# Performance work log

Hardware: AMD Instinct MI355X
Metric: run time of the kernel (lower is better)

Reference implementation:

```python
import jax, jax.numpy as jnp
import numpy as np
import math

B, T, C = 4, 2048, 1024
H, D = 16, 64            # num_heads, head_dim
ORIG_LEN = 4096
MIN_FREQ, MAX_FREQ = 0.5, 40.0


def setup_inputs() -> dict:
    key = jax.random.key(0)
    ks = jax.random.split(key, 6)
    x = jax.random.normal(ks[0], (B, T, C), dtype=jnp.float32)
    keep_idx = jnp.sort(jax.random.randint(ks[1], (B, T, 1), 0, ORIG_LEN), axis=1)
    W_qkv = jax.random.normal(ks[2], (C, 3 * C), dtype=jnp.float32) * (1.0 / math.sqrt(C))
    b_qkv = jnp.zeros((3 * C,), dtype=jnp.float32)
    W_proj = jax.random.normal(ks[3], (C, C), dtype=jnp.float32) * (1.0 / math.sqrt(C))
    b_proj = jnp.zeros((C,), dtype=jnp.float32)
    return {"x": x, "keep_idx": keep_idx, "original_seq_len": ORIG_LEN,
            "W_qkv": W_qkv, "b_qkv": b_qkv, "W_proj": W_proj, "b_proj": b_proj}


def _rope_angles(positions, orig_len):
    # positions: [b, t] float token positions in the ORIGINAL sequence.
    # golden_gate 1-D RoPE: normalized positions times geometric frequency band.
    half = D // 2
    freqs = MIN_FREQ * (MAX_FREQ / MIN_FREQ) ** (jnp.arange(half, dtype=jnp.float32) / (half - 1))
    pos_norm = positions / jnp.float32(orig_len)          # [b, t]
    return 2.0 * jnp.pi * pos_norm[:, :, None] * freqs    # [b, t, half]


def _apply_rope(x, cos, sin):
    # x: [b, h, t, d]; cos/sin: [b, 1, t, d/2]; rotate (first half, second half) pairs
    half = D // 2
    x1, x2 = x[..., :half], x[..., half:]
    return jnp.concatenate([x1 * cos - x2 * sin, x1 * sin + x2 * cos], axis=-1)


def reference(x, keep_idx, original_seq_len, W_qkv, b_qkv, W_proj, b_proj):
    b, t, c = x.shape
    # fused QKV projection + head split: (b,t,3c) -> (b,t,3,h,d) -> (b,h,t,3,d)
    qkv = (x @ W_qkv + b_qkv).reshape(b, t, 3, H, D).transpose(0, 3, 1, 2, 4)
    q, k, v = qkv[:, :, :, 0], qkv[:, :, :, 1], qkv[:, :, :, 2]  # each [b,h,t,d]

    positions = keep_idx[..., 0].astype(jnp.float32)             # [b, t]
    ang = _rope_angles(positions, original_seq_len)              # [b, t, d/2]
    cos = jnp.cos(ang)[:, None]                                  # [b,1,t,d/2]
    sin = jnp.sin(ang)[:, None]
    q = _apply_rope(q, cos, sin)
    k = _apply_rope(k, cos, sin)

    # dense non-causal scaled dot-product attention
    scale = 1.0 / math.sqrt(D)
    scores = jnp.einsum('bhqd,bhkd->bhqk', q, k) * scale
    attn = jax.nn.softmax(scores, axis=-1)
    out = jnp.einsum('bhqk,bhkd->bhqd', attn, v)                 # [b,h,t,d]

    out = out.transpose(0, 2, 1, 3).reshape(b, t, H * D)         # [b,t,c]
    return out @ W_proj + b_proj
```

## Files before the change

### kernel.cpp

```cpp
#include <hip/hip_runtime.h>
#include <hip/hip_bf16.h>
#include <math.h>

#define B_ 4
#define T_ 2048
#define C_ 1024
#define H_ 16
#define D_ 64

typedef __attribute__((ext_vector_type(8))) short bf16x8_t;
typedef __attribute__((ext_vector_type(4))) float f32x4_t;
typedef __attribute__((ext_vector_type(2))) unsigned int uiv2_t;

#define SHIFT2 32.0f

#define GLOAD_LDS16(gp, lp)                                                          \
    __builtin_amdgcn_global_load_lds(                                                \
        (const __attribute__((address_space(1))) void*)(gp),                         \
        (__attribute__((address_space(3))) void*)(lp), 16, 0, 0)

#define WAVE_ORDER() __builtin_amdgcn_wave_barrier()

__device__ inline short bf16bits(float f) {
    __hip_bfloat16 h = __float2bfloat16(f);
    return *reinterpret_cast<short*>(&h);
}

__device__ inline unsigned int pack2bf(float a, float b) {
    __hip_bfloat162 h = __float22bfloat162_rn(make_float2(a, b));
    return *reinterpret_cast<unsigned int*>(&h);
}

__global__ void xconv_kernel(const float* __restrict__ in,
                             __hip_bfloat16* __restrict__ out, int n4) {
    int i = blockIdx.x * blockDim.x + threadIdx.x;
    if (i < n4) {
        float4 v = *(const float4*)(in + (size_t)i * 4);
        uint2 u;
        u.x = pack2bf(v.x, v.y);
        u.y = pack2bf(v.z, v.w);
        *(uint2*)(out + (size_t)i * 4) = u;
    }
}

__global__ void rope_tab_kernel(const int* __restrict__ keep,
                                const int* __restrict__ orig,
                                float* __restrict__ tab) {
    int i = blockIdx.x * blockDim.x + threadIdx.x;
    int tok = i >> 5, d = i & 31;
    float freq = 0.5f * exp2f((float)d * (6.321928094887362f / 31.0f));
    float ang  = 6.283185307179586f * ((float)keep[tok] / (float)(*orig)) * freq;
    tab[(size_t)tok * 64 + d]      = cosf(ang);
    tab[(size_t)tok * 64 + 32 + d] = sinf(ang);
}

__global__ void transpose_conv_kernel(const float* __restrict__ in,
                                      __hip_bfloat16* __restrict__ out,
                                      int K, int N) {
    __shared__ float s[32][33];
    const int n0 = blockIdx.x * 32;
    const int k0 = blockIdx.y * 32;
    const int tx = threadIdx.x;
    const int ty = threadIdx.y;
#pragma unroll
    for (int yy = 0; yy < 32; yy += 8)
        s[ty + yy][tx] = in[(size_t)(k0 + ty + yy) * N + n0 + tx];
    __syncthreads();
#pragma unroll
    for (int yy = 0; yy < 32; yy += 8)
        out[(size_t)(n0 + ty + yy) * K + k0 + tx] = __float2bfloat16(s[tx][ty + yy]);
}

#define GTILE (128 * 32)

template <int MODE>
__global__ __launch_bounds__(256)
void gemm_kernel(const __hip_bfloat16* __restrict__ A,
                 const __hip_bfloat16* __restrict__ BT,
                 const float* __restrict__ bias,
                 float* __restrict__ out,
                 __hip_bfloat16* __restrict__ qbuf,
                 __hip_bfloat16* __restrict__ kbuf,
                 __hip_bfloat16* __restrict__ vtbuf,
                 const float* __restrict__ ropetab,
                 int M, int N, int K) {
    __shared__ __align__(16) __hip_bfloat16 As[2 * GTILE];
    __shared__ __align__(16) __hip_bfloat16 Bs[2 * GTILE];

    const int tid  = threadIdx.x;
    const int lane = tid & 63;
    const int wave = tid >> 6;
    const int wm   = wave >> 1;
    const int wn   = wave & 1;
    const int l15  = lane & 15;
    const int quad = lane >> 4;

    const int nT  = N >> 7;
    const int grp = blockIdx.x / (8 * nT);
    const int rem = blockIdx.x - grp * 8 * nT;
    const int m0  = (grp * 8 + (rem & 7)) * 128;
    const int n0  = (rem >> 3) * 128;

    f32x4_t acc[4][4];
#pragma unroll
    for (int i = 0; i < 4; i++)
#pragma unroll
        for (int j = 0; j < 4; j++) acc[i][j] = (f32x4_t)0.0f;

    const int lrow = lane >> 2;
    const int lcol = (lane & 3) * 8;
    const __hip_bfloat16* gA  = A  + (size_t)(m0 + wave * 16 + lrow) * K + lcol;
    const __hip_bfloat16* gA2 = gA + (size_t)64 * K;
    const __hip_bfloat16* gB  = BT + (size_t)(n0 + wave * 16 + lrow) * K + lcol;
    const __hip_bfloat16* gB2 = gB + (size_t)64 * K;
    const int ldsW = wave * 16 * 32;

    GLOAD_LDS16(gA,  As + ldsW);
    GLOAD_LDS16(gA2, As + ldsW + 64 * 32);
    GLOAD_LDS16(gB,  Bs + ldsW);
    GLOAD_LDS16(gB2, Bs + ldsW + 64 * 32);

    const int NK = K >> 5;
    for (int t = 0; t < NK; ++t) {
        const int off = (t & 1) * GTILE;
        if (t + 1 < NK) {
            const int noff = off ^ GTILE;
            const int kk   = (t + 1) << 5;
            GLOAD_LDS16(gA  + kk, As + noff + ldsW);
            GLOAD_LDS16(gA2 + kk, As + noff + ldsW + 64 * 32);
            GLOAD_LDS16(gB  + kk, Bs + noff + ldsW);
            GLOAD_LDS16(gB2 + kk, Bs + noff + ldsW + 64 * 32);
            asm volatile("s_waitcnt vmcnt(4)" ::: "memory");
        } else {
            asm volatile("s_waitcnt vmcnt(0)" ::: "memory");
        }
        __builtin_amdgcn_s_barrier();
        __builtin_amdgcn_sched_barrier(0);

        bf16x8_t af[4], bfv[4];
#pragma unroll
        for (int i = 0; i < 4; i++)
            af[i] = *(const bf16x8_t*)(As + off + (wm * 64 + i * 16 + l15) * 32 + quad * 8);
#pragma unroll
        for (int j = 0; j < 4; j++)
            bfv[j] = *(const bf16x8_t*)(Bs + off + (wn * 64 + j * 16 + l15) * 32 + quad * 8);
#pragma unroll
        for (int i = 0; i < 4; i++)
#pragma unroll
            for (int j = 0; j < 4; j++)
                acc[i][j] = __builtin_amdgcn_mfma_f32_16x16x32_bf16(af[i], bfv[j], acc[i][j], 0, 0, 0);

        __builtin_amdgcn_sched_barrier(0);
        asm volatile("s_waitcnt lgkmcnt(0)" ::: "memory");
        __builtin_amdgcn_s_barrier();
    }

    float bv[4];
#pragma unroll
    for (int j = 0; j < 4; j++)
        bv[j] = bias[n0 + wn * 64 + j * 16 + l15];

    if (MODE == 0) {
#pragma unroll
        for (int i = 0; i < 4; i++)
#pragma unroll
            for (int r = 0; r < 4; r++) {
                int row = m0 + wm * 64 + i * 16 + quad * 4 + r;
#pragma unroll
                for (int j = 0; j < 4; j++) {
                    int col = n0 + wn * 64 + j * 16 + l15;
                    out[(size_t)row * N + col] = acc[i][j][r] + bv[j];
                }
            }
    } else {
        const int cb   = n0 + wn * 64;
        const int part = cb >> 10;
        const int h    = (cb & 1023) >> 6;
        if (part == 2) {
#pragma unroll
            for (int j = 0; j < 4; j++) {
#pragma unroll
                for (int i = 0; i < 4; i++) {
#pragma unroll
                    for (int r = 0; r < 4; r++) {
                        int row = m0 + wm * 64 + i * 16 + quad * 4 + r;
                        int b = row >> 11;
                        int t = row & 2047;
                        int d = j * 16 + l15;
                        vtbuf[((size_t)((b * H_ + h) * D_ + d)) * T_ + t] =
                            __float2bfloat16(acc[i][j][r] + bv[j]);
                    }
                }
            }
        } else {
            __hip_bfloat16* dst = (part == 0) ? qbuf : kbuf;
            const float sc = (part == 0) ? 0.18033688011112042f : 1.0f;
#pragma unroll
            for (int i = 0; i < 4; i++) {
#pragma unroll
                for (int r = 0; r < 4; r++) {
                    int row = m0 + wm * 64 + i * 16 + quad * 4 + r;
                    int b = row >> 11;
                    int t = row & 2047;
                    const float* trow = ropetab + (size_t)row * 64;
                    size_t base = ((size_t)(b * H_ + h) * T_ + t) * D_;
#pragma unroll
                    for (int j = 0; j < 2; j++) {
                        int d = j * 16 + l15;
                        float cs = trow[d];
                        float sn = trow[32 + d];
                        float x1 = acc[i][j][r]     + bv[j];
                        float x2 = acc[i][j + 2][r] + bv[j + 2];
                        dst[base + d]      = __float2bfloat16(sc * (x1 * cs - x2 * sn));
                        dst[base + d + 32] = __float2bfloat16(sc * (x1 * sn + x2 * cs));
                    }
                }
            }
        }
    }
}

#define KVTILE (64 * 64)

__global__ __launch_bounds__(256, 4)
void attn_kernel(const __hip_bfloat16* __restrict__ q,
                 const __hip_bfloat16* __restrict__ k,
                 const __hip_bfloat16* __restrict__ vt,
                 __hip_bfloat16* __restrict__ attn_out) {
    __shared__ __align__(16) __hip_bfloat16 SMEM[4 * KVTILE];

    const int tid  = threadIdx.x;
    const int lane = tid & 63;
    const int wave = tid >> 6;
    const int l15  = lane & 15;
    const int quad = lane >> 4;
    const int x7   = l15 & 7;

    const int bh = blockIdx.x & 63;
    const int qt = blockIdx.x >> 6;
    const int b  = bh >> 4;
    const int h  = bh & 15;

    const size_t qkbase = (size_t)bh * T_ * D_;
    const size_t vbase  = (size_t)bh * D_ * T_;
    const int    qrow0  = qt * 128 + wave * 32;

    const int drow   = lane >> 3;
    const int gchunk = (lane & 7) ^ drow;

    const __hip_bfloat16* kg = k + qkbase;
    const __hip_bfloat16* vg = vt + vbase;

    const int c0 = ((quad)     ^ x7) * 8;
    const int c1 = ((4 + quad) ^ x7) * 8;

    bf16x8_t qa[2][2];
#pragma unroll
    for (int qf = 0; qf < 2; qf++)
#pragma unroll
        for (int kk = 0; kk < 2; kk++)
            qa[qf][kk] = *(const bf16x8_t*)(q + qkbase +
                          (size_t)(qrow0 + qf * 16 + l15) * D_ + kk * 32 + quad * 8);

    bf16x8_t ones;
#pragma unroll
    for (int i = 0; i < 8; i++) ones[i] = (short)0x3F80;

    const f32x4_t mbias = (f32x4_t)(-SHIFT2);

    f32x4_t o[2][4];
#pragma unroll
    for (int qf = 0; qf < 2; qf++)
#pragma unroll
        for (int jd = 0; jd < 4; jd++) o[qf][jd] = (f32x4_t)0.0f;
    f32x4_t osum[2];
    osum[0] = (f32x4_t)0.0f;
    osum[1] = (f32x4_t)0.0f;

#pragma unroll
    for (int i = 0; i < 2; i++) {
        int r = wave * 16 + i * 8;
        GLOAD_LDS16(kg + (size_t)(r + drow) * D_ + gchunk * 8, SMEM + r * 64);
        GLOAD_LDS16(vg + (size_t)(r + drow) * T_ + gchunk * 8, SMEM + 2 * KVTILE + r * 64);
    }

    for (int kt = 0; kt < T_ / 64; kt++) {
        const int curoff = (kt & 1) * KVTILE;
        const int nxtoff = curoff ^ KVTILE;
        if (kt + 1 < T_ / 64) {
#pragma unroll
            for (int i = 0; i < 2; i++) {
                int r = wave * 16 + i * 8;
                GLOAD_LDS16(kg + (size_t)((kt + 1) * 64 + r + drow) * D_ + gchunk * 8,
                            SMEM + nxtoff + r * 64);
                GLOAD_LDS16(vg + (size_t)(r + drow) * T_ + (kt + 1) * 64 + gchunk * 8,
                            SMEM + 2 * KVTILE + nxtoff + r * 64);
            }
            asm volatile("s_waitcnt vmcnt(4)" ::: "memory");
        } else {
            asm volatile("s_waitcnt vmcnt(0)" ::: "memory");
        }
        __builtin_amdgcn_s_barrier();
        __builtin_amdgcn_sched_barrier(0);

        const __hip_bfloat16* KLc = SMEM + curoff;
        const __hip_bfloat16* VLc = SMEM + 2 * KVTILE + curoff;

        bf16x8_t kf[4][2];
#pragma unroll
        for (int jt = 0; jt < 4; jt++) {
            kf[jt][0] = *(const bf16x8_t*)(KLc + (jt * 16 + l15) * 64 + c0);
            kf[jt][1] = *(const bf16x8_t*)(KLc + (jt * 16 + l15) * 64 + c1);
        }

        f32x4_t sT[2][4];
        __builtin_amdgcn_s_setprio(1);
#pragma unroll
        for (int jt = 0; jt < 4; jt++)
#pragma unroll
            for (int qf = 0; qf < 2; qf++) {
                sT[qf][jt] = __builtin_amdgcn_mfma_f32_16x16x32_bf16(
                    kf[jt][0], qa[qf][0], mbias, 0, 0, 0);
                sT[qf][jt] = __builtin_amdgcn_mfma_f32_16x16x32_bf16(
                    kf[jt][1], qa[qf][1], sT[qf][jt], 0, 0, 0);
            }
        __builtin_amdgcn_s_setprio(0);

        bf16x8_t pb[2][2];
#pragma unroll
        for (int qf = 0; qf < 2; qf++) {
            unsigned int w0[4], w1[4];
#pragma unroll
            for (int jt = 0; jt < 4; jt++) {
                float p0 = __builtin_amdgcn_exp2f(sT[qf][jt][0]);
                float p1 = __builtin_amdgcn_exp2f(sT[qf][jt][1]);
                float p2 = __builtin_amdgcn_exp2f(sT[qf][jt][2]);
                float p3 = __builtin_amdgcn_exp2f(sT[qf][jt][3]);
                w0[jt] = pack2bf(p0, p1);
                w1[jt] = pack2bf(p2, p3);
            }
#pragma unroll
            for (int kk = 0; kk < 2; kk++) {
                uiv2_t s0 = __builtin_amdgcn_permlane32_swap(w0[2 * kk], w0[2 * kk + 1], false, false);
                uiv2_t r0 = __builtin_amdgcn_permlane16_swap(s0[0], s0[1], false, false);
                uiv2_t s1 = __builtin_amdgcn_permlane32_swap(w1[2 * kk], w1[2 * kk + 1], false, false);
                uiv2_t r1 = __builtin_amdgcn_permlane16_swap(s1[0], s1[1], false, false);
                union { unsigned int u[4]; bf16x8_t v; } pu;
                pu.u[0] = r0[0];
                pu.u[1] = r1[0];
                pu.u[2] = r0[1];
                pu.u[3] = r1[1];
                pb[qf][kk] = pu.v;
            }
        }

        __builtin_amdgcn_s_setprio(1);
#pragma unroll
        for (int qf = 0; qf < 2; qf++) {
            osum[qf] = __builtin_amdgcn_mfma_f32_16x16x32_bf16(ones, pb[qf][0], osum[qf], 0, 0, 0);
            osum[qf] = __builtin_amdgcn_mfma_f32_16x16x32_bf16(ones, pb[qf][1], osum[qf], 0, 0, 0);
        }

#pragma unroll
        for (int jd = 0; jd < 4; jd++) {
            bf16x8_t vf0 = *(const bf16x8_t*)(VLc + (jd * 16 + l15) * 64 + c0);
            bf16x8_t vf1 = *(const bf16x8_t*)(VLc + (jd * 16 + l15) * 64 + c1);
#pragma unroll
            for (int qf = 0; qf < 2; qf++) {
                o[qf][jd] = __builtin_amdgcn_mfma_f32_16x16x32_bf16(vf0, pb[qf][0], o[qf][jd], 0, 0, 0);
                o[qf][jd] = __builtin_amdgcn_mfma_f32_16x16x32_bf16(vf1, pb[qf][1], o[qf][jd], 0, 0, 0);
            }
        }
        __builtin_amdgcn_s_setprio(0);

        __builtin_amdgcn_sched_barrier(0);
        asm volatile("s_waitcnt lgkmcnt(0)" ::: "memory");
        __builtin_amdgcn_s_barrier();
    }

    float inv[2];
    inv[0] = 1.0f / osum[0][0];
    inv[1] = 1.0f / osum[1][0];

    __hip_bfloat16* Pep = SMEM + wave * (32 * 72);

    WAVE_ORDER();
#pragma unroll
    for (int qf = 0; qf < 2; qf++) {
#pragma unroll
        for (int jd = 0; jd < 4; jd++) {
            uint2 pk;
            pk.x = pack2bf(o[qf][jd][0] * inv[qf], o[qf][jd][1] * inv[qf]);
            pk.y = pack2bf(o[qf][jd][2] * inv[qf], o[qf][jd][3] * inv[qf]);
            *(uint2*)(Pep + (qf * 16 + l15) * 72 + jd * 16 + quad * 4) = pk;
        }
    }
    WAVE_ORDER();

#pragma unroll
    for (int rnd = 0; rnd < 4; rnd++) {
        int row = rnd * 8 + (lane >> 3);
        int col = (lane & 7) * 8;
        bf16x8_t vrow = *(const bf16x8_t*)(Pep + row * 72 + col);
        int token = qt * 128 + wave * 32 + row;
        *(bf16x8_t*)(attn_out + ((size_t)(b * T_ + token)) * C_ + h * 64 + col) = vrow;
    }
}

extern "C" void kernel_launch(void* const* d_in, const int* in_sizes, int n_in,
                              void* d_out, int out_size, void* d_ws, size_t ws_size,
                              hipStream_t stream) {
    const float* x        = (const float*)d_in[0];
    const int*   keep_idx = (const int*)d_in[1];
    const int*   orig_len = (const int*)d_in[2];
    const float* Wqkv     = (const float*)d_in[3];
    const float* bqkv     = (const float*)d_in[4];
    const float* Wproj    = (const float*)d_in[5];
    const float* bproj    = (const float*)d_in[6];
    float*       out      = (float*)d_out;

    const size_t NTOK = (size_t)B_ * T_;
    const size_t QKV1 = NTOK * C_;

    __hip_bfloat16* qbuf    = (__hip_bfloat16*)d_ws;
    __hip_bfloat16* kbuf    = qbuf    + QKV1;
    __hip_bfloat16* vtbuf   = kbuf    + QKV1;
    __hip_bfloat16* attnbuf = vtbuf   + QKV1;
    __hip_bfloat16* WqkvT   = attnbuf + QKV1;
    __hip_bfloat16* WprojT  = WqkvT   + (size_t)C_ * 3 * C_;
    __hip_bfloat16* xbf     = WprojT  + (size_t)C_ * C_;
    float*          ropetab = (float*)(xbf + QKV1);

    xconv_kernel<<<(QKV1 / 4 + 255) / 256, 256, 0, stream>>>(x, xbf, (int)(QKV1 / 4));
    rope_tab_kernel<<<(NTOK * 32) / 256, 256, 0, stream>>>(keep_idx, orig_len, ropetab);

    dim3 tb(32, 8);
    transpose_conv_kernel<<<dim3(3 * C_ / 32, C_ / 32), tb, 0, stream>>>(Wqkv, WqkvT, C_, 3 * C_);
    transpose_conv_kernel<<<dim3(C_ / 32, C_ / 32), tb, 0, stream>>>(Wproj, WprojT, C_, C_);

    gemm_kernel<1><<<(8192 / 128) * (3072 / 128), 256, 0, stream>>>(
        xbf, WqkvT, bqkv, nullptr, qbuf, kbuf, vtbuf, ropetab, 8192, 3072, 1024);

    attn_kernel<<<(T_ / 128) * 64, 256, 0, stream>>>(qbuf, kbuf, vtbuf, attnbuf);

    gemm_kernel<0><<<(8192 / 128) * (1024 / 128), 256, 0, stream>>>(
        attnbuf, WprojT, bproj, out, nullptr, nullptr, nullptr, nullptr, 8192, 1024, 1024);
}
```

Measured before the change: 296.8 us.

## Triple-buffer GEMM LDS with XOR swizzle and stage V-transpose through LDS

The GEMM main loop moves from double to triple buffering, so global-to-LDS loads run two k-tiles ahead with a deeper vmcnt wait. The LDS tile layout is XOR-swizzled on both the global_load_lds write side and the MFMA fragment read side to cut bank conflicts. The V-transpose epilogue now stages the tile in shared memory and writes vtbuf with contiguous 16-byte stores instead of strided scalar stores. LDS use grows from 4 to 6 tiles, which may lower occupancy, and the epilogue adds a block-wide sync.

```diff
diff --git a/kernel.cpp b/kernel.cpp
--- a/kernel.cpp
+++ b/kernel.cpp
@@ -84,8 +84,7 @@
                  __hip_bfloat16* __restrict__ vtbuf,
                  const float* __restrict__ ropetab,
                  int M, int N, int K) {
-    __shared__ __align__(16) __hip_bfloat16 As[2 * GTILE];
-    __shared__ __align__(16) __hip_bfloat16 Bs[2 * GTILE];
+    __shared__ __align__(16) __hip_bfloat16 GS[6 * GTILE];
 
     const int tid  = threadIdx.x;
     const int lane = tid & 63;
@@ -108,28 +107,37 @@
         for (int j = 0; j < 4; j++) acc[i][j] = (f32x4_t)0.0f;
 
     const int lrow = lane >> 2;
-    const int lcol = (lane & 3) * 8;
-    const __hip_bfloat16* gA  = A  + (size_t)(m0 + wave * 16 + lrow) * K + lcol;
+    const int scol = ((lane & 3) ^ ((lane >> 4) & 3)) * 8;
+    const __hip_bfloat16* gA  = A  + (size_t)(m0 + wave * 16 + lrow) * K + scol;
     const __hip_bfloat16* gA2 = gA + (size_t)64 * K;
-    const __hip_bfloat16* gB  = BT + (size_t)(n0 + wave * 16 + lrow) * K + lcol;
+    const __hip_bfloat16* gB  = BT + (size_t)(n0 + wave * 16 + lrow) * K + scol;
     const __hip_bfloat16* gB2 = gB + (size_t)64 * K;
     const int ldsW = wave * 16 * 32;
 
-    GLOAD_LDS16(gA,  As + ldsW);
-    GLOAD_LDS16(gA2, As + ldsW + 64 * 32);
-    GLOAD_LDS16(gB,  Bs + ldsW);
-    GLOAD_LDS16(gB2, Bs + ldsW + 64 * 32);
-
     const int NK = K >> 5;
+    GLOAD_LDS16(gA,  GS + ldsW);
+    GLOAD_LDS16(gA2, GS + ldsW + 64 * 32);
+    GLOAD_LDS16(gB,  GS + 3 * GTILE + ldsW);
+    GLOAD_LDS16(gB2, GS + 3 * GTILE + ldsW + 64 * 32);
+    if (NK > 1) {
+        GLOAD_LDS16(gA  + 32, GS + GTILE + ldsW);
+        GLOAD_LDS16(gA2 + 32, GS + GTILE + ldsW + 64 * 32);
+        GLOAD_LDS16(gB  + 32, GS + 3 * GTILE + GTILE + ldsW);
+        GLOAD_LDS16(gB2 + 32, GS + 3 * GTILE + GTILE + ldsW + 64 * 32);
+    }
+
+    int off = 0;
     for (int t = 0; t < NK; ++t) {
-        const int off = (t & 1) * GTILE;
-        if (t + 1 < NK) {
-            const int noff = off ^ GTILE;
-            const int kk   = (t + 1) << 5;
-            GLOAD_LDS16(gA  + kk, As + noff + ldsW);
-            GLOAD_LDS16(gA2 + kk, As + noff + ldsW + 64 * 32);
-            GLOAD_LDS16(gB  + kk, Bs + noff + ldsW);
-            GLOAD_LDS16(gB2 + kk, Bs + noff + ldsW + 64 * 32);
+        if (t + 2 < NK) {
+            int poff = off + 2 * GTILE;
+            if (poff >= 3 * GTILE) poff -= 3 * GTILE;
+            const int kk = (t + 2) << 5;
+            GLOAD_LDS16(gA  + kk, GS + poff + ldsW);
+            GLOAD_LDS16(gA2 + kk, GS + poff + ldsW + 64 * 32);
+            GLOAD_LDS16(gB  + kk, GS + 3 * GTILE + poff + ldsW);
+            GLOAD_LDS16(gB2 + kk, GS + 3 * GTILE + poff + ldsW + 64 * 32);
+            asm volatile("s_waitcnt vmcnt(8)" ::: "memory");
+        } else if (t + 1 < NK) {
             asm volatile("s_waitcnt vmcnt(4)" ::: "memory");
         } else {
             asm volatile("s_waitcnt vmcnt(0)" ::: "memory");
@@ -140,10 +148,12 @@
         bf16x8_t af[4], bfv[4];
 #pragma unroll
         for (int i = 0; i < 4; i++)
-            af[i] = *(const bf16x8_t*)(As + off + (wm * 64 + i * 16 + l15) * 32 + quad * 8);
+            af[i] = *(const bf16x8_t*)(GS + off + (wm * 64 + i * 16 + l15) * 32 +
+                                       ((quad ^ (l15 >> 2)) * 8));
 #pragma unroll
         for (int j = 0; j < 4; j++)
-            bfv[j] = *(const bf16x8_t*)(Bs + off + (wn * 64 + j * 16 + l15) * 32 + quad * 8);
+            bfv[j] = *(const bf16x8_t*)(GS + 3 * GTILE + off + (wn * 64 + j * 16 + l15) * 32 +
+                                        ((quad ^ (l15 >> 2)) * 8));
 #pragma unroll
         for (int i = 0; i < 4; i++)
 #pragma unroll
@@ -153,6 +163,9 @@
         __builtin_amdgcn_sched_barrier(0);
         asm volatile("s_waitcnt lgkmcnt(0)" ::: "memory");
         __builtin_amdgcn_s_barrier();
+
+        off += GTILE;
+        if (off == 3 * GTILE) off = 0;
     }
 
     float bv[4];
@@ -175,24 +188,35 @@
     } else {
         const int cb   = n0 + wn * 64;
         const int part = cb >> 10;
-        const int h    = (cb & 1023) >> 6;
         if (part == 2) {
-#pragma unroll
-            for (int j = 0; j < 4; j++) {
-#pragma unroll
-                for (int i = 0; i < 4; i++) {
+            const int hb = (n0 & 1023) >> 6;
+            __hip_bfloat16* myL = GS + wn * (64 * 136);
+#pragma unroll
+            for (int j = 0; j < 4; j++)
+#pragma unroll
+                for (int i = 0; i < 4; i++)
 #pragma unroll
                     for (int r = 0; r < 4; r++) {
-                        int row = m0 + wm * 64 + i * 16 + quad * 4 + r;
-                        int b = row >> 11;
-                        int t = row & 2047;
-                        int d = j * 16 + l15;
-                        vtbuf[((size_t)((b * H_ + h) * D_ + d)) * T_ + t] =
-                            __float2bfloat16(acc[i][j][r] + bv[j]);
+                        int rt = wm * 64 + i * 16 + quad * 4 + r;
+                        int d  = j * 16 + l15;
+                        myL[d * 136 + rt] = __float2bfloat16(acc[i][j][r] + bv[j]);
                     }
-                }
+            __syncthreads();
+            const int bb  = m0 >> 11;
+            const int t0  = m0 & 2047;
+            const int row = tid >> 1;
+            const int wn2 = row >> 6;
+            const int dd  = row & 63;
+            const __hip_bfloat16* src = GS + wn2 * (64 * 136) + dd * 136;
+            __hip_bfloat16* dstv = vtbuf +
+                ((size_t)((bb * H_ + hb + wn2) * D_ + dd)) * T_ + t0;
+#pragma unroll
+            for (int s = 0; s < 8; s++) {
+                int ch = (tid & 1) * 8 + s;
+                *(bf16x8_t*)(dstv + ch * 8) = *(const bf16x8_t*)(src + ch * 8);
             }
         } else {
+            const int h = (cb & 1023) >> 6;
             __hip_bfloat16* dst = (part == 0) ? qbuf : kbuf;
             const float sc = (part == 0) ? 0.18033688011112042f : 1.0f;
 #pragma unroll
```

New measurement: 269.9 us. 9.1% less time.
